# Kernel tuning notes

Hardware: AMD Instinct MI355X
Metric: run time of the kernel (lower is better)

The kernel has to match this reference:

```python
import jax, jax.numpy as jnp
import numpy as np


def setup_inputs() -> dict:
    key = jax.random.key(0)
    kx, kt = jax.random.split(key)
    Q, N, D = 2048, 100000, 256
    x = jax.random.normal(kx, (Q, D), dtype=jnp.float32)
    training_data = jax.random.normal(kt, (N, D), dtype=jnp.float32)
    return {"x": x, "training_data": training_data, "k": 16}


def _euclidean_cdist(x, y):
    x2 = jnp.sum(x * x, axis=1, keepdims=True)            # [Q, 1]
    y2 = jnp.sum(y * y, axis=1)[None, :]                  # [1, N]
    d2 = x2 - 2.0 * (x @ y.T) + y2                        # [Q, N]
    return jnp.sqrt(jnp.maximum(d2, 0.0))


def reference(x, training_data, k):
    # KNN.forward: full pairwise euclidean distances, then k smallest (sorted ascending)
    distances = _euclidean_cdist(x, training_data)        # [Q, N]
    _, indices = jax.lax.top_k(-distances, k)             # smallest distances
    return indices                                        # [Q, k] int32
```

## Files before the change

kernel.cpp:

```cpp
#include <hip/hip_runtime.h>
#include <math.h>

#define D_DIM 256
#define KSEL  16
#define BQ    64
#define BN    64
#define DK    32
#define CHUNK 1600
#define NTILES (CHUNK / BN)
#define LDP   68

#define XS_OFF 0
#define YS_OFF (DK * LDP)
#define SC_OFF (2 * DK * LDP)
#define SMEM_WORDS (SC_OFF + BQ * LDP)
#define MD_OFF 0
#define MI_OFF 4352

__device__ __forceinline__ bool pair_less(float a, int ia, float b, int ib) {
    return (a < b) || (a == b && ia < ib);
}

#define INSERT_CAND(sval, ival)                                              \
    do {                                                                     \
        _Pragma("unroll")                                                    \
        for (int jj = KSEL - 1; jj >= 1; --jj) {                             \
            bool cj  = pair_less((sval), (ival), bd[jj], bi[jj]);            \
            bool cj1 = pair_less((sval), (ival), bd[jj - 1], bi[jj - 1]);    \
            bd[jj] = cj ? (cj1 ? bd[jj - 1] : (sval)) : bd[jj];              \
            bi[jj] = cj ? (cj1 ? bi[jj - 1] : (ival)) : bi[jj];              \
        }                                                                    \
        if (pair_less((sval), (ival), bd[0], bi[0])) {                       \
            bd[0] = (sval); bi[0] = (ival);                                  \
        }                                                                    \
    } while (0)

__global__ __launch_bounds__(256) void knn_y2(const float* __restrict__ y,
                                              float* __restrict__ y2, int N) {
    int gw   = (blockIdx.x * 256 + threadIdx.x) >> 6;
    int lane = threadIdx.x & 63;
    if (gw >= N) return;
    const float4 v =
        *reinterpret_cast<const float4*>(y + (size_t)gw * D_DIM + lane * 4);
    float s = v.x * v.x + v.y * v.y + v.z * v.z + v.w * v.w;
#pragma unroll
    for (int off = 32; off > 0; off >>= 1) s += __shfl_down(s, off, 64);
    if (lane == 0) y2[gw] = s;
}

__global__ __launch_bounds__(256) void knn_phase1(
    const float* __restrict__ x, const float* __restrict__ y,
    const float* __restrict__ y2, float* __restrict__ pd,
    int* __restrict__ pi, int N, int S) {
    __shared__ float smem[SMEM_WORDS];

    const int tid   = threadIdx.x;
    const int qbase = blockIdx.x * BQ;
    const int chunk = blockIdx.y;
    const int tq    = tid >> 4;
    const int tn    = tid & 15;
    const int q     = tid & 63;
    const int part  = tid >> 6;

    float bd[KSEL];
    int   bi[KSEL];
#pragma unroll
    for (int j = 0; j < KSEL; ++j) { bd[j] = __builtin_inff(); bi[j] = 0x7fffffff; }

    const int sr   = tid >> 3;
    const int scol = (tid & 7) * 4;

    for (int t = 0; t < NTILES; ++t) {
        const int nbase = chunk * CHUNK + t * BN;

        float acc[4][4];
#pragma unroll
        for (int i = 0; i < 4; ++i)
#pragma unroll
            for (int j = 0; j < 4; ++j) acc[i][j] = 0.0f;

        for (int dk = 0; dk < D_DIM; dk += DK) {
            __syncthreads();
#pragma unroll
            for (int h = 0; h < 2; ++h) {
                const int rr = sr + h * 32;
                const float4 xv = *reinterpret_cast<const float4*>(
                    x + (size_t)(qbase + rr) * D_DIM + dk + scol);
                smem[XS_OFF + (scol + 0) * LDP + rr] = xv.x;
                smem[XS_OFF + (scol + 1) * LDP + rr] = xv.y;
                smem[XS_OFF + (scol + 2) * LDP + rr] = xv.z;
                smem[XS_OFF + (scol + 3) * LDP + rr] = xv.w;

                const int yr = nbase + rr;
                float4 yv = make_float4(0.f, 0.f, 0.f, 0.f);
                if (yr < N)
                    yv = *reinterpret_cast<const float4*>(
                        y + (size_t)yr * D_DIM + dk + scol);
                smem[YS_OFF + (scol + 0) * LDP + rr] = yv.x;
                smem[YS_OFF + (scol + 1) * LDP + rr] = yv.y;
                smem[YS_OFF + (scol + 2) * LDP + rr] = yv.z;
                smem[YS_OFF + (scol + 3) * LDP + rr] = yv.w;
            }
            __syncthreads();

#pragma unroll
            for (int d = 0; d < DK; ++d) {
                const float4 xa = *reinterpret_cast<const float4*>(
                    &smem[XS_OFF + d * LDP + tq * 4]);
                const float4 yb = *reinterpret_cast<const float4*>(
                    &smem[YS_OFF + d * LDP + tn * 4]);
                acc[0][0] = fmaf(xa.x, yb.x, acc[0][0]);
                acc[0][1] = fmaf(xa.x, yb.y, acc[0][1]);
                acc[0][2] = fmaf(xa.x, yb.z, acc[0][2]);
                acc[0][3] = fmaf(xa.x, yb.w, acc[0][3]);
                acc[1][0] = fmaf(xa.y, yb.x, acc[1][0]);
                acc[1][1] = fmaf(xa.y, yb.y, acc[1][1]);
                acc[1][2] = fmaf(xa.y, yb.z, acc[1][2]);
                acc[1][3] = fmaf(xa.y, yb.w, acc[1][3]);
                acc[2][0] = fmaf(xa.z, yb.x, acc[2][0]);
                acc[2][1] = fmaf(xa.z, yb.y, acc[2][1]);
                acc[2][2] = fmaf(xa.z, yb.z, acc[2][2]);
                acc[2][3] = fmaf(xa.z, yb.w, acc[2][3]);
                acc[3][0] = fmaf(xa.w, yb.x, acc[3][0]);
                acc[3][1] = fmaf(xa.w, yb.y, acc[3][1]);
                acc[3][2] = fmaf(xa.w, yb.z, acc[3][2]);
                acc[3][3] = fmaf(xa.w, yb.w, acc[3][3]);
            }
        }

        float yv2[4];
#pragma unroll
        for (int j = 0; j < 4; ++j) {
            const int gn = nbase + tn * 4 + j;
            yv2[j] = (gn < N) ? y2[gn] : 0.0f;
        }
#pragma unroll
        for (int i = 0; i < 4; ++i) {
            const int qq = tq * 4 + i;
            float4 sv;
            sv.x = (nbase + tn * 4 + 0 < N) ? fmaf(-2.0f, acc[i][0], yv2[0])
                                            : __builtin_inff();
            sv.y = (nbase + tn * 4 + 1 < N) ? fmaf(-2.0f, acc[i][1], yv2[1])
                                            : __builtin_inff();
            sv.z = (nbase + tn * 4 + 2 < N) ? fmaf(-2.0f, acc[i][2], yv2[2])
                                            : __builtin_inff();
            sv.w = (nbase + tn * 4 + 3 < N) ? fmaf(-2.0f, acc[i][3], yv2[3])
                                            : __builtin_inff();
            *reinterpret_cast<float4*>(&smem[SC_OFF + qq * LDP + tn * 4]) = sv;
        }
        __syncthreads();

        {
            const float* scrow = &smem[SC_OFF + q * LDP + part * 16];
#pragma unroll 1
            for (int j0 = 0; j0 < 16; ++j0) {
                const int jc = (j0 + q) & 15;
                const int gn = nbase + part * 16 + jc;
                const float s = scrow[jc];
                if (gn < N && pair_less(s, gn, bd[KSEL - 1], bi[KSEL - 1])) {
                    INSERT_CAND(s, gn);
                }
            }
        }
        __syncthreads();
    }

    {
        float* md = &smem[MD_OFF];
        int*   mi = (int*)&smem[MI_OFF];
#pragma unroll
        for (int j = 0; j < KSEL; ++j) {
            md[(part * BQ + q) * 17 + j] = bd[j];
            mi[(part * BQ + q) * 17 + j] = bi[j];
        }
        __syncthreads();
        if (tid < BQ) {
#pragma unroll 1
            for (int p = 1; p < 4; ++p) {
#pragma unroll 1
                for (int j = 0; j < KSEL; ++j) {
                    const float v  = md[(p * BQ + tid) * 17 + j];
                    const int   id = mi[(p * BQ + tid) * 17 + j];
                    if (!pair_less(v, id, bd[KSEL - 1], bi[KSEL - 1])) break;
                    INSERT_CAND(v, id);
                }
            }
            const size_t base = ((size_t)(qbase + tid) * S + chunk) * KSEL;
#pragma unroll
            for (int j = 0; j < KSEL; ++j) {
                pd[base + j] = bd[j];
                pi[base + j] = bi[j];
            }
        }
    }
}

__global__ __launch_bounds__(256) void knn_phase2(const float* __restrict__ pd,
                                                  const int* __restrict__ pi,
                                                  int* __restrict__ out, int S,
                                                  int Qtot) {
    const int q = blockIdx.x * 256 + threadIdx.x;
    if (q >= Qtot) return;

    float bd[KSEL];
    int   bi[KSEL];
#pragma unroll
    for (int j = 0; j < KSEL; ++j) { bd[j] = __builtin_inff(); bi[j] = 0x7fffffff; }

#pragma unroll 1
    for (int c = 0; c < S; ++c) {
        const float* pdl = pd + ((size_t)q * S + c) * KSEL;
        const int*   pil = pi + ((size_t)q * S + c) * KSEL;
#pragma unroll 1
        for (int j = 0; j < KSEL; ++j) {
            const float v  = pdl[j];
            const int   id = pil[j];
            if (!pair_less(v, id, bd[KSEL - 1], bi[KSEL - 1])) break;
            INSERT_CAND(v, id);
        }
    }

#pragma unroll
    for (int j = 0; j < KSEL; ++j) out[q * KSEL + j] = bi[j];
}

extern "C" void kernel_launch(void* const* d_in, const int* in_sizes, int n_in,
                              void* d_out, int out_size, void* d_ws,
                              size_t ws_size, hipStream_t stream) {
    const float* x = (const float*)d_in[0];
    const float* y = (const float*)d_in[1];
    int* out = (int*)d_out;

    const int Q = in_sizes[0] / D_DIM;
    const int N = in_sizes[1] / D_DIM;
    const int S = (N + CHUNK - 1) / CHUNK;

    float* y2 = (float*)d_ws;
    float* pd = y2 + N;
    int*   pi = (int*)(pd + (size_t)Q * S * KSEL);

    knn_y2<<<(N * 64 + 255) / 256, 256, 0, stream>>>(y, y2, N);
    knn_phase1<<<dim3(Q / BQ, S), 256, 0, stream>>>(x, y, y2, pd, pi, N, S);
    knn_phase2<<<(Q + 255) / 256, 256, 0, stream>>>(pd, pi, out, S, Q);
}
```

Baseline: 4.074 ms.

## Double-buffer shared-memory tiles with register prefetch across K-steps and tiles

Restructures the distance GEMM inner loop into a software pipeline. The global loads for the next DK slice, or for the first slice of the next N tile, are issued into registers before computing on the current shared buffer, then written into the alternate buffer. This halves the barriers per K-step and hides global-load latency behind the FMAs. The score tile is aliased onto the second buffer to keep shared-memory use the same, which depends on careful ordering of when that buffer is live.

```diff
diff --git a/kernel.cpp b/kernel.cpp
--- a/kernel.cpp
+++ b/kernel.cpp
@@ -10,10 +10,10 @@
 #define NTILES (CHUNK / BN)
 #define LDP   68
 
-#define XS_OFF 0
-#define YS_OFF (DK * LDP)
-#define SC_OFF (2 * DK * LDP)
-#define SMEM_WORDS (SC_OFF + BQ * LDP)
+#define XS_W      (DK * LDP)
+#define BUF_WORDS (2 * XS_W)
+#define SC_OFF    BUF_WORDS
+#define SMEM_WORDS (2 * BUF_WORDS)
 #define MD_OFF 0
 #define MI_OFF 4352
 
@@ -70,63 +70,45 @@
     const int sr   = tid >> 3;
     const int scol = (tid & 7) * 4;
 
+    const float4 fzero = make_float4(0.f, 0.f, 0.f, 0.f);
+    float4 xpf0, xpf1, ypf0, ypf1;
+
+    {
+        const int nb = chunk * CHUNK;
+        xpf0 = *reinterpret_cast<const float4*>(
+            x + (size_t)(qbase + sr) * D_DIM + scol);
+        xpf1 = *reinterpret_cast<const float4*>(
+            x + (size_t)(qbase + sr + 32) * D_DIM + scol);
+        const int yr0 = nb + sr, yr1 = nb + sr + 32;
+        ypf0 = (yr0 < N) ? *reinterpret_cast<const float4*>(
+                               y + (size_t)yr0 * D_DIM + scol)
+                         : fzero;
+        ypf1 = (yr1 < N) ? *reinterpret_cast<const float4*>(
+                               y + (size_t)yr1 * D_DIM + scol)
+                         : fzero;
+        float* xs = smem;
+        float* ys = smem + XS_W;
+        xs[(scol + 0) * LDP + sr] = xpf0.x;
+        xs[(scol + 1) * LDP + sr] = xpf0.y;
+        xs[(scol + 2) * LDP + sr] = xpf0.z;
+        xs[(scol + 3) * LDP + sr] = xpf0.w;
+        xs[(scol + 0) * LDP + sr + 32] = xpf1.x;
+        xs[(scol + 1) * LDP + sr + 32] = xpf1.y;
+        xs[(scol + 2) * LDP + sr + 32] = xpf1.z;
+        xs[(scol + 3) * LDP + sr + 32] = xpf1.w;
+        ys[(scol + 0) * LDP + sr] = ypf0.x;
+        ys[(scol + 1) * LDP + sr] = ypf0.y;
+        ys[(scol + 2) * LDP + sr] = ypf0.z;
+        ys[(scol + 3) * LDP + sr] = ypf0.w;
+        ys[(scol + 0) * LDP + sr + 32] = ypf1.x;
+        ys[(scol + 1) * LDP + sr + 32] = ypf1.y;
+        ys[(scol + 2) * LDP + sr + 32] = ypf1.z;
+        ys[(scol + 3) * LDP + sr + 32] = ypf1.w;
+    }
+    __syncthreads();
+
     for (int t = 0; t < NTILES; ++t) {
         const int nbase = chunk * CHUNK + t * BN;
-
-        float acc[4][4];
-#pragma unroll
-        for (int i = 0; i < 4; ++i)
-#pragma unroll
-            for (int j = 0; j < 4; ++j) acc[i][j] = 0.0f;
-
-        for (int dk = 0; dk < D_DIM; dk += DK) {
-            __syncthreads();
-#pragma unroll
-            for (int h = 0; h < 2; ++h) {
-                const int rr = sr + h * 32;
-                const float4 xv = *reinterpret_cast<const float4*>(
-                    x + (size_t)(qbase + rr) * D_DIM + dk + scol);
-                smem[XS_OFF + (scol + 0) * LDP + rr] = xv.x;
-                smem[XS_OFF + (scol + 1) * LDP + rr] = xv.y;
-                smem[XS_OFF + (scol + 2) * LDP + rr] = xv.z;
-                smem[XS_OFF + (scol + 3) * LDP + rr] = xv.w;
-
-                const int yr = nbase + rr;
-                float4 yv = make_float4(0.f, 0.f, 0.f, 0.f);
-                if (yr < N)
-                    yv = *reinterpret_cast<const float4*>(
-                        y + (size_t)yr * D_DIM + dk + scol);
-                smem[YS_OFF + (scol + 0) * LDP + rr] = yv.x;
-                smem[YS_OFF + (scol + 1) * LDP + rr] = yv.y;
-                smem[YS_OFF + (scol + 2) * LDP + rr] = yv.z;
-                smem[YS_OFF + (scol + 3) * LDP + rr] = yv.w;
-            }
-            __syncthreads();
-
-#pragma unroll
-            for (int d = 0; d < DK; ++d) {
-                const float4 xa = *reinterpret_cast<const float4*>(
-                    &smem[XS_OFF + d * LDP + tq * 4]);
-                const float4 yb = *reinterpret_cast<const float4*>(
-                    &smem[YS_OFF + d * LDP + tn * 4]);
-                acc[0][0] = fmaf(xa.x, yb.x, acc[0][0]);
-                acc[0][1] = fmaf(xa.x, yb.y, acc[0][1]);
-                acc[0][2] = fmaf(xa.x, yb.z, acc[0][2]);
-                acc[0][3] = fmaf(xa.x, yb.w, acc[0][3]);
-                acc[1][0] = fmaf(xa.y, yb.x, acc[1][0]);
-                acc[1][1] = fmaf(xa.y, yb.y, acc[1][1]);
-                acc[1][2] = fmaf(xa.y, yb.z, acc[1][2]);
-                acc[1][3] = fmaf(xa.y, yb.w, acc[1][3]);
-                acc[2][0] = fmaf(xa.z, yb.x, acc[2][0]);
-                acc[2][1] = fmaf(xa.z, yb.y, acc[2][1]);
-                acc[2][2] = fmaf(xa.z, yb.z, acc[2][2]);
-                acc[2][3] = fmaf(xa.z, yb.w, acc[2][3]);
-                acc[3][0] = fmaf(xa.w, yb.x, acc[3][0]);
-                acc[3][1] = fmaf(xa.w, yb.y, acc[3][1]);
-                acc[3][2] = fmaf(xa.w, yb.z, acc[3][2]);
-                acc[3][3] = fmaf(xa.w, yb.w, acc[3][3]);
-            }
-        }
 
         float yv2[4];
 #pragma unroll
@@ -134,19 +116,101 @@
             const int gn = nbase + tn * 4 + j;
             yv2[j] = (gn < N) ? y2[gn] : 0.0f;
         }
-#pragma unroll
-        for (int i = 0; i < 4; ++i) {
-            const int qq = tq * 4 + i;
-            float4 sv;
-            sv.x = (nbase + tn * 4 + 0 < N) ? fmaf(-2.0f, acc[i][0], yv2[0])
-                                            : __builtin_inff();
-            sv.y = (nbase + tn * 4 + 1 < N) ? fmaf(-2.0f, acc[i][1], yv2[1])
-                                            : __builtin_inff();
-            sv.z = (nbase + tn * 4 + 2 < N) ? fmaf(-2.0f, acc[i][2], yv2[2])
-                                            : __builtin_inff();
-            sv.w = (nbase + tn * 4 + 3 < N) ? fmaf(-2.0f, acc[i][3], yv2[3])
-                                            : __builtin_inff();
-            *reinterpret_cast<float4*>(&smem[SC_OFF + qq * LDP + tn * 4]) = sv;
+
+        float acc[4][4];
+#pragma unroll
+        for (int i = 0; i < 4; ++i)
+#pragma unroll
+            for (int j = 0; j < 4; ++j) acc[i][j] = 0.0f;
+
+        for (int s = 0; s < 8; ++s) {
+            const int p = s & 1;
+            const bool has_next = !(t == NTILES - 1 && s == 7);
+
+            if (has_next) {
+                const int ns  = (s < 7) ? s + 1 : 0;
+                const int ndk = ns * DK;
+                const int nnb = (s < 7) ? nbase : nbase + BN;
+                xpf0 = *reinterpret_cast<const float4*>(
+                    x + (size_t)(qbase + sr) * D_DIM + ndk + scol);
+                xpf1 = *reinterpret_cast<const float4*>(
+                    x + (size_t)(qbase + sr + 32) * D_DIM + ndk + scol);
+                const int yr0 = nnb + sr, yr1 = nnb + sr + 32;
+                ypf0 = (yr0 < N) ? *reinterpret_cast<const float4*>(
+                                       y + (size_t)yr0 * D_DIM + ndk + scol)
+                                 : fzero;
+                ypf1 = (yr1 < N) ? *reinterpret_cast<const float4*>(
+                                       y + (size_t)yr1 * D_DIM + ndk + scol)
+                                 : fzero;
+            }
+
+            {
+                const float* xs = smem + p * BUF_WORDS;
+                const float* ys = xs + XS_W;
+#pragma unroll
+                for (int d = 0; d < DK; ++d) {
+                    const float4 xa = *reinterpret_cast<const float4*>(
+                        &xs[d * LDP + tq * 4]);
+                    const float4 yb = *reinterpret_cast<const float4*>(
+                        &ys[d * LDP + tn * 4]);
+                    acc[0][0] = fmaf(xa.x, yb.x, acc[0][0]);
+                    acc[0][1] = fmaf(xa.x, yb.y, acc[0][1]);
+                    acc[0][2] = fmaf(xa.x, yb.z, acc[0][2]);
+                    acc[0][3] = fmaf(xa.x, yb.w, acc[0][3]);
+                    acc[1][0] = fmaf(xa.y, yb.x, acc[1][0]);
+                    acc[1][1] = fmaf(xa.y, yb.y, acc[1][1]);
+                    acc[1][2] = fmaf(xa.y, yb.z, acc[1][2]);
+                    acc[1][3] = fmaf(xa.y, yb.w, acc[1][3]);
+                    acc[2][0] = fmaf(xa.z, yb.x, acc[2][0]);
+                    acc[2][1] = fmaf(xa.z, yb.y, acc[2][1]);
+                    acc[2][2] = fmaf(xa.z, yb.z, acc[2][2]);
+                    acc[2][3] = fmaf(xa.z, yb.w, acc[2][3]);
+                    acc[3][0] = fmaf(xa.w, yb.x, acc[3][0]);
+                    acc[3][1] = fmaf(xa.w, yb.y, acc[3][1]);
+                    acc[3][2] = fmaf(xa.w, yb.z, acc[3][2]);
+                    acc[3][3] = fmaf(xa.w, yb.w, acc[3][3]);
+                }
+            }
+
+            if (has_next) {
+                float* xs = smem + (p ^ 1) * BUF_WORDS;
+                float* ys = xs + XS_W;
+                xs[(scol + 0) * LDP + sr] = xpf0.x;
+                xs[(scol + 1) * LDP + sr] = xpf0.y;
+                xs[(scol + 2) * LDP + sr] = xpf0.z;
+                xs[(scol + 3) * LDP + sr] = xpf0.w;
+                xs[(scol + 0) * LDP + sr + 32] = xpf1.x;
+                xs[(scol + 1) * LDP + sr + 32] = xpf1.y;
+                xs[(scol + 2) * LDP + sr + 32] = xpf1.z;
+                xs[(scol + 3) * LDP + sr + 32] = xpf1.w;
+                ys[(scol + 0) * LDP + sr] = ypf0.x;
+                ys[(scol + 1) * LDP + sr] = ypf0.y;
+                ys[(scol + 2) * LDP + sr] = ypf0.z;
+                ys[(scol + 3) * LDP + sr] = ypf0.w;
+                ys[(scol + 0) * LDP + sr + 32] = ypf1.x;
+                ys[(scol + 1) * LDP + sr + 32] = ypf1.y;
+                ys[(scol + 2) * LDP + sr + 32] = ypf1.z;
+                ys[(scol + 3) * LDP + sr + 32] = ypf1.w;
+            }
+            __syncthreads();
+        }
+
+        {
+            float* sc = smem + SC_OFF;
+#pragma unroll
+            for (int i = 0; i < 4; ++i) {
+                const int qq = tq * 4 + i;
+                float4 sv;
+                sv.x = (nbase + tn * 4 + 0 < N) ? fmaf(-2.0f, acc[i][0], yv2[0])
+                                                : __builtin_inff();
+                sv.y = (nbase + tn * 4 + 1 < N) ? fmaf(-2.0f, acc[i][1], yv2[1])
+                                                : __builtin_inff();
+                sv.z = (nbase + tn * 4 + 2 < N) ? fmaf(-2.0f, acc[i][2], yv2[2])
+                                                : __builtin_inff();
+                sv.w = (nbase + tn * 4 + 3 < N) ? fmaf(-2.0f, acc[i][3], yv2[3])
+                                                : __builtin_inff();
+                *reinterpret_cast<float4*>(&sc[qq * LDP + tn * 4]) = sv;
+            }
         }
         __syncthreads();
 
```

New measurement: 6.099 ms. 49.7% more time.

## Enlarge distance tile to 128x128 with 8x8 per-thread micro-tiles and two-lane selection

Applied to the files above, without the earlier changes.

Raises the block tile from 64x64 to 128x128 queries by points, with each thread computing an 8x8 register micro-tile over DK=16 slices. This raises arithmetic intensity and cuts shared-memory traffic per FMA. Top-k selection now runs in two halves through a 64-row score buffer, with two threads per query each scanning 64 columns, and the final merge combines two partial lists instead of four. The 64 accumulators plus the top-k registers raise register pressure, which may reduce occupancy. The chunk size per block also changes, which shifts the grid shape and the phase-2 merge width.

```diff
diff --git a/kernel.cpp b/kernel.cpp
--- a/kernel.cpp
+++ b/kernel.cpp
@@ -3,18 +3,17 @@
 
 #define D_DIM 256
 #define KSEL  16
-#define BQ    64
-#define BN    64
-#define DK    32
-#define CHUNK 1600
-#define NTILES (CHUNK / BN)
-#define LDP   68
+#define BQ    128
+#define BN    128
+#define DK    16
+#define NT    13
+#define CHUNK (NT * BN)
+#define LDP   132
 
 #define XS_OFF 0
 #define YS_OFF (DK * LDP)
 #define SC_OFF (2 * DK * LDP)
-#define SMEM_WORDS (SC_OFF + BQ * LDP)
-#define MD_OFF 0
+#define SMEM_WORDS (SC_OFF + 64 * LDP)
 #define MI_OFF 4352
 
 __device__ __forceinline__ bool pair_less(float a, int ia, float b, int ib) {
@@ -59,131 +58,155 @@
     const int chunk = blockIdx.y;
     const int tq    = tid >> 4;
     const int tn    = tid & 15;
-    const int q     = tid & 63;
-    const int part  = tid >> 6;
+    const int srow  = tid >> 1;
+    const int sdh   = (tid & 1) * 8;
+    const int sq    = tid >> 1;
+    const int spart = tid & 1;
+    const int sql   = sq & 63;
+    const int sqh   = sq >> 6;
 
     float bd[KSEL];
     int   bi[KSEL];
 #pragma unroll
     for (int j = 0; j < KSEL; ++j) { bd[j] = __builtin_inff(); bi[j] = 0x7fffffff; }
 
-    const int sr   = tid >> 3;
-    const int scol = (tid & 7) * 4;
-
-    for (int t = 0; t < NTILES; ++t) {
+    for (int t = 0; t < NT; ++t) {
         const int nbase = chunk * CHUNK + t * BN;
 
-        float acc[4][4];
-#pragma unroll
-        for (int i = 0; i < 4; ++i)
-#pragma unroll
-            for (int j = 0; j < 4; ++j) acc[i][j] = 0.0f;
-
-        for (int dk = 0; dk < D_DIM; dk += DK) {
-            __syncthreads();
-#pragma unroll
-            for (int h = 0; h < 2; ++h) {
-                const int rr = sr + h * 32;
-                const float4 xv = *reinterpret_cast<const float4*>(
-                    x + (size_t)(qbase + rr) * D_DIM + dk + scol);
-                smem[XS_OFF + (scol + 0) * LDP + rr] = xv.x;
-                smem[XS_OFF + (scol + 1) * LDP + rr] = xv.y;
-                smem[XS_OFF + (scol + 2) * LDP + rr] = xv.z;
-                smem[XS_OFF + (scol + 3) * LDP + rr] = xv.w;
-
-                const int yr = nbase + rr;
-                float4 yv = make_float4(0.f, 0.f, 0.f, 0.f);
-                if (yr < N)
-                    yv = *reinterpret_cast<const float4*>(
-                        y + (size_t)yr * D_DIM + dk + scol);
-                smem[YS_OFF + (scol + 0) * LDP + rr] = yv.x;
-                smem[YS_OFF + (scol + 1) * LDP + rr] = yv.y;
-                smem[YS_OFF + (scol + 2) * LDP + rr] = yv.z;
-                smem[YS_OFF + (scol + 3) * LDP + rr] = yv.w;
+        float yv2[8];
+#pragma unroll
+        for (int j = 0; j < 8; ++j) {
+            const int gn = nbase + tn * 8 + j;
+            yv2[j] = (gn < N) ? y2[gn] : 0.0f;
+        }
+
+        float acc[8][8];
+#pragma unroll
+        for (int i = 0; i < 8; ++i)
+#pragma unroll
+            for (int j = 0; j < 8; ++j) acc[i][j] = 0.0f;
+
+        for (int ks = 0; ks < D_DIM / DK; ++ks) {
+            const int dk = ks * DK;
+            __syncthreads();
+            {
+                const float4 gx0 = *reinterpret_cast<const float4*>(
+                    x + (size_t)(qbase + srow) * D_DIM + dk + sdh);
+                const float4 gx1 = *reinterpret_cast<const float4*>(
+                    x + (size_t)(qbase + srow) * D_DIM + dk + sdh + 4);
+                float* xs = smem + XS_OFF;
+                xs[(sdh + 0) * LDP + srow] = gx0.x;
+                xs[(sdh + 1) * LDP + srow] = gx0.y;
+                xs[(sdh + 2) * LDP + srow] = gx0.z;
+                xs[(sdh + 3) * LDP + srow] = gx0.w;
+                xs[(sdh + 4) * LDP + srow] = gx1.x;
+                xs[(sdh + 5) * LDP + srow] = gx1.y;
+                xs[(sdh + 6) * LDP + srow] = gx1.z;
+                xs[(sdh + 7) * LDP + srow] = gx1.w;
+
+                const int gn = nbase + srow;
+                float4 gy0 = make_float4(0.f, 0.f, 0.f, 0.f), gy1 = gy0;
+                if (gn < N) {
+                    gy0 = *reinterpret_cast<const float4*>(
+                        y + (size_t)gn * D_DIM + dk + sdh);
+                    gy1 = *reinterpret_cast<const float4*>(
+                        y + (size_t)gn * D_DIM + dk + sdh + 4);
+                }
+                float* ys = smem + YS_OFF;
+                ys[(sdh + 0) * LDP + srow] = gy0.x;
+                ys[(sdh + 1) * LDP + srow] = gy0.y;
+                ys[(sdh + 2) * LDP + srow] = gy0.z;
+                ys[(sdh + 3) * LDP + srow] = gy0.w;
+                ys[(sdh + 4) * LDP + srow] = gy1.x;
+                ys[(sdh + 5) * LDP + srow] = gy1.y;
+                ys[(sdh + 6) * LDP + srow] = gy1.z;
+                ys[(sdh + 7) * LDP + srow] = gy1.w;
             }
             __syncthreads();
 
 #pragma unroll
             for (int d = 0; d < DK; ++d) {
-                const float4 xa = *reinterpret_cast<const float4*>(
-                    &smem[XS_OFF + d * LDP + tq * 4]);
-                const float4 yb = *reinterpret_cast<const float4*>(
-                    &smem[YS_OFF + d * LDP + tn * 4]);
-                acc[0][0] = fmaf(xa.x, yb.x, acc[0][0]);
-                acc[0][1] = fmaf(xa.x, yb.y, acc[0][1]);
-                acc[0][2] = fmaf(xa.x, yb.z, acc[0][2]);
-                acc[0][3] = fmaf(xa.x, yb.w, acc[0][3]);
-                acc[1][0] = fmaf(xa.y, yb.x, acc[1][0]);
-                acc[1][1] = fmaf(xa.y, yb.y, acc[1][1]);
-                acc[1][2] = fmaf(xa.y, yb.z, acc[1][2]);
-                acc[1][3] = fmaf(xa.y, yb.w, acc[1][3]);
-                acc[2][0] = fmaf(xa.z, yb.x, acc[2][0]);
-                acc[2][1] = fmaf(xa.z, yb.y, acc[2][1]);
-                acc[2][2] = fmaf(xa.z, yb.z, acc[2][2]);
-                acc[2][3] = fmaf(xa.z, yb.w, acc[2][3]);
-                acc[3][0] = fmaf(xa.w, yb.x, acc[3][0]);
-                acc[3][1] = fmaf(xa.w, yb.y, acc[3][1]);
-                acc[3][2] = fmaf(xa.w, yb.z, acc[3][2]);
-                acc[3][3] = fmaf(xa.w, yb.w, acc[3][3]);
-            }
-        }
-
-        float yv2[4];
-#pragma unroll
-        for (int j = 0; j < 4; ++j) {
-            const int gn = nbase + tn * 4 + j;
-            yv2[j] = (gn < N) ? y2[gn] : 0.0f;
-        }
-#pragma unroll
-        for (int i = 0; i < 4; ++i) {
-            const int qq = tq * 4 + i;
-            float4 sv;
-            sv.x = (nbase + tn * 4 + 0 < N) ? fmaf(-2.0f, acc[i][0], yv2[0])
-                                            : __builtin_inff();
-            sv.y = (nbase + tn * 4 + 1 < N) ? fmaf(-2.0f, acc[i][1], yv2[1])
-                                            : __builtin_inff();
-            sv.z = (nbase + tn * 4 + 2 < N) ? fmaf(-2.0f, acc[i][2], yv2[2])
-                                            : __builtin_inff();
-            sv.w = (nbase + tn * 4 + 3 < N) ? fmaf(-2.0f, acc[i][3], yv2[3])
-                                            : __builtin_inff();
-            *reinterpret_cast<float4*>(&smem[SC_OFF + qq * LDP + tn * 4]) = sv;
-        }
-        __syncthreads();
-
-        {
-            const float* scrow = &smem[SC_OFF + q * LDP + part * 16];
-#pragma unroll 1
-            for (int j0 = 0; j0 < 16; ++j0) {
-                const int jc = (j0 + q) & 15;
-                const int gn = nbase + part * 16 + jc;
-                const float s = scrow[jc];
-                if (gn < N && pair_less(s, gn, bd[KSEL - 1], bi[KSEL - 1])) {
-                    INSERT_CAND(s, gn);
+                const float4 xa0 = *reinterpret_cast<const float4*>(
+                    &smem[XS_OFF + d * LDP + tq * 8]);
+                const float4 xa1 = *reinterpret_cast<const float4*>(
+                    &smem[XS_OFF + d * LDP + tq * 8 + 4]);
+                const float4 yb0 = *reinterpret_cast<const float4*>(
+                    &smem[YS_OFF + d * LDP + tn * 8]);
+                const float4 yb1 = *reinterpret_cast<const float4*>(
+                    &smem[YS_OFF + d * LDP + tn * 8 + 4]);
+                const float xv[8] = {xa0.x, xa0.y, xa0.z, xa0.w,
+                                     xa1.x, xa1.y, xa1.z, xa1.w};
+                const float yv[8] = {yb0.x, yb0.y, yb0.z, yb0.w,
+                                     yb1.x, yb1.y, yb1.z, yb1.w};
+#pragma unroll
+                for (int i = 0; i < 8; ++i)
+#pragma unroll
+                    for (int j = 0; j < 8; ++j)
+                        acc[i][j] = fmaf(xv[i], yv[j], acc[i][j]);
+            }
+        }
+
+#pragma unroll 1
+        for (int h = 0; h < 2; ++h) {
+            if ((tq >> 3) == h) {
+                float* sc = smem + SC_OFF;
+                const int lr0 = (tq & 7) * 8;
+#pragma unroll
+                for (int i = 0; i < 8; ++i) {
+                    float4 s0, s1;
+                    s0.x = (nbase + tn * 8 + 0 < N) ? fmaf(-2.f, acc[i][0], yv2[0]) : __builtin_inff();
+                    s0.y = (nbase + tn * 8 + 1 < N) ? fmaf(-2.f, acc[i][1], yv2[1]) : __builtin_inff();
+                    s0.z = (nbase + tn * 8 + 2 < N) ? fmaf(-2.f, acc[i][2], yv2[2]) : __builtin_inff();
+                    s0.w = (nbase + tn * 8 + 3 < N) ? fmaf(-2.f, acc[i][3], yv2[3]) : __builtin_inff();
+                    s1.x = (nbase + tn * 8 + 4 < N) ? fmaf(-2.f, acc[i][4], yv2[4]) : __builtin_inff();
+                    s1.y = (nbase + tn * 8 + 5 < N) ? fmaf(-2.f, acc[i][5], yv2[5]) : __builtin_inff();
+                    s1.z = (nbase + tn * 8 + 6 < N) ? fmaf(-2.f, acc[i][6], yv2[6]) : __builtin_inff();
+                    s1.w = (nbase + tn * 8 + 7 < N) ? fmaf(-2.f, acc[i][7], yv2[7]) : __builtin_inff();
+                    *reinterpret_cast<float4*>(&sc[(lr0 + i) * LDP + tn * 8]) = s0;
+                    *reinterpret_cast<float4*>(&sc[(lr0 + i) * LDP + tn * 8 + 4]) = s1;
                 }
             }
-        }
-        __syncthreads();
+            __syncthreads();
+            if (sqh == h) {
+                const float* scrow = &smem[SC_OFF + sql * LDP];
+#pragma unroll 1
+                for (int s = 0; s < 64; ++s) {
+                    const int w   = (s + sql + spart) & 63;
+                    const int col = spart * 64 + w;
+                    const int gn  = nbase + col;
+                    const float sval = scrow[col];
+                    if (gn < N && sval <= bd[KSEL - 1]) {
+                        INSERT_CAND(sval, gn);
+                    }
+                }
+            }
+            __syncthreads();
+        }
     }
 
     {
-        float* md = &smem[MD_OFF];
+        float* md = smem;
         int*   mi = (int*)&smem[MI_OFF];
+        const int lid = sq * 2 + spart;
 #pragma unroll
         for (int j = 0; j < KSEL; ++j) {
-            md[(part * BQ + q) * 17 + j] = bd[j];
-            mi[(part * BQ + q) * 17 + j] = bi[j];
+            md[lid * 17 + j] = bd[j];
+            mi[lid * 17 + j] = bi[j];
         }
         __syncthreads();
         if (tid < BQ) {
-#pragma unroll 1
-            for (int p = 1; p < 4; ++p) {
-#pragma unroll 1
-                for (int j = 0; j < KSEL; ++j) {
-                    const float v  = md[(p * BQ + tid) * 17 + j];
-                    const int   id = mi[(p * BQ + tid) * 17 + j];
-                    if (!pair_less(v, id, bd[KSEL - 1], bi[KSEL - 1])) break;
-                    INSERT_CAND(v, id);
-                }
+            const float* l0d = &md[(tid * 2) * 17];
+            const int*   l0i = &mi[(tid * 2) * 17];
+#pragma unroll
+            for (int j = 0; j < KSEL; ++j) { bd[j] = l0d[j]; bi[j] = l0i[j]; }
+            const float* l1d = &md[(tid * 2 + 1) * 17];
+            const int*   l1i = &mi[(tid * 2 + 1) * 17];
+#pragma unroll 1
+            for (int j = 0; j < KSEL; ++j) {
+                const float v  = l1d[j];
+                const int   id = l1i[j];
+                if (!pair_less(v, id, bd[KSEL - 1], bi[KSEL - 1])) break;
+                INSERT_CAND(v, id);
             }
             const size_t base = ((size_t)(qbase + tid) * S + chunk) * KSEL;
 #pragma unroll
```

After: 8.150 ms. 2x slower.
